# Kernel tuning notes

Measured on AMD Instinct MI355X. Metric: run time of the kernel, lower is better.

Reference implementation:

```python
import jax, jax.numpy as jnp
import numpy as np

NUM_HEADS = 12
T_TASK = 0  # current task index (training uses prompts[:, t:t+1])


def setup_inputs() -> dict:
    key = jax.random.key(0)
    ks = jax.random.split(key, 6)
    B, N, C = 64, 197, 768
    G = 8            # num_selectors
    P = 8            # num_prompts
    NT = 10          # num_tasks
    hd = C // NUM_HEADS
    return {
        "x": jax.random.normal(ks[0], (B, N, C), dtype=jnp.float32),
        "tokens": jax.random.normal(ks[1], (1, B, 1 + G, C), dtype=jnp.float32),
        "qkv_w": jax.random.normal(ks[2], (3 * C, C), dtype=jnp.float32) * 0.02,
        "proj_w": jax.random.normal(ks[3], (C, C), dtype=jnp.float32) * 0.02,
        "proj_b": jax.random.normal(ks[4], (C,), dtype=jnp.float32) * 0.02,
        "prompts": jax.random.normal(ks[5], (2, NT, P, NUM_HEADS, hd), dtype=jnp.float32),
    }


def _forward(x, tokens, qkv_w, proj_w, proj_b, prompts):
    C = x.shape[-1]
    hd = C // NUM_HEADS
    scale = hd ** -0.5
    token_scale = C ** -0.5

    # ---- selector cross-attention (x detached) ----
    xd = jax.lax.stop_gradient(x)
    task_cls = tokens[:, :, 0:1]        # [T,B,1,C]
    selectors = tokens[:, :, 1:]        # [T,B,G,C]
    g_attn = jnp.einsum('tbsc,bnc->tbsn', selectors, xd) * token_scale
    g_soft = jax.nn.softmax(g_attn, axis=-1)
    task_patches = jnp.einsum('bnc,tbsn->tbsc', xd, g_soft)
    task_x = jnp.concatenate([task_cls, task_patches], axis=2)  # [T,B,H,C]
    T, B, H, _ = task_x.shape

    # ---- prompt-augmented task attention ----
    qkv = (task_x @ qkv_w.T).reshape(T, B, H, 3, NUM_HEADS, hd)
    qkv = qkv.transpose(3, 0, 1, 4, 2, 5)          # [3,T,B,heads,H,hd]
    q, k, v = qkv[0], qkv[1], qkv[2]

    pr = prompts[:, T_TASK:T_TASK + 1]             # [2,1,P,heads,hd] (training slice)
    P = pr.shape[2]
    pr = jnp.broadcast_to(pr[:, :, None], (2, 1, B, P, NUM_HEADS, hd))
    pr = pr.transpose(0, 1, 2, 4, 3, 5)            # [2,1,B,heads,P,hd]
    k = jnp.concatenate([pr[0], k], axis=-2)       # [T,B,heads,P+H,hd]
    v = jnp.concatenate([pr[1], v], axis=-2)

    attn = jax.nn.softmax((q @ jnp.swapaxes(k, -2, -1)) * scale, axis=-1)
    out = jnp.swapaxes(attn @ v, 2, 3).reshape(T, B, H, C)
    task_out = out @ proj_w.T + proj_b

    # disable_dandr == False, tome == 0 -> keep selectors, replace cls
    tokens_out = jnp.concatenate([task_out[:, :, 0:1], selectors], axis=2)

    # ---- frozen standard patch attention (no_grad) ----
    Bn, N, _ = x.shape
    qkv2 = (xd @ qkv_w.T).reshape(Bn, N, 3, NUM_HEADS, hd).transpose(2, 0, 3, 1, 4)
    q2, k2, v2 = qkv2[0], qkv2[1], qkv2[2]
    a2 = jax.nn.softmax((q2 @ jnp.swapaxes(k2, -2, -1)) * scale, axis=-1)
    xo = jnp.swapaxes(a2 @ v2, 1, 2).reshape(Bn, N, C)
    xo = jax.lax.stop_gradient(xo @ proj_w.T + proj_b)
    return xo, tokens_out


def reference(x, tokens, qkv_w, proj_w, proj_b, prompts):
    return _forward(x, tokens, qkv_w, proj_w, proj_b, prompts)
```

## Files before the change

### kernel.cpp

```cpp
#include <hip/hip_runtime.h>
#include <hip/hip_bf16.h>
#include <cstddef>
#include <cstdint>


typedef __attribute__((ext_vector_type(8))) short    bf16x8;
typedef __attribute__((ext_vector_type(8))) unsigned short ushort8;
typedef __attribute__((ext_vector_type(4))) unsigned short ushort4v;
typedef __attribute__((ext_vector_type(4))) float    f32x4;

__device__ __forceinline__ unsigned short f2bf_rne(float f) {
    unsigned int u = __float_as_uint(f);
    u += 0x7fff + ((u >> 16) & 1);
    return (unsigned short)(u >> 16);
}
__device__ __forceinline__ float bf2f(unsigned short h) {
    return __uint_as_float(((unsigned int)h) << 16);
}

__global__ __launch_bounds__(256)
void split_hl_kernel(const float* __restrict__ in, unsigned short* __restrict__ hi,
                     unsigned short* __restrict__ lo, int n4)
{
    int i = blockIdx.x * 256 + threadIdx.x;
    const int stride = gridDim.x * 256;
    for (; i < n4; i += stride) {
        float4 v = ((const float4*)in)[i];
        float f[4] = {v.x, v.y, v.z, v.w};
        ushort4v h4, l4;
#pragma unroll
        for (int j = 0; j < 4; ++j) {
            unsigned short hh = f2bf_rne(f[j]);
            h4[j] = hh;
            l4[j] = f2bf_rne(f[j] - bf2f(hh));
        }
        ((ushort4v*)hi)[i] = h4;
        ((ushort4v*)lo)[i] = l4;
    }
}

__global__ __launch_bounds__(256)
void gemm_hl_kernel(const unsigned short* __restrict__ Ah_g, const unsigned short* __restrict__ Al_g,
                    const unsigned short* __restrict__ Bh_g, const unsigned short* __restrict__ Bl_g,
                    const float* __restrict__ bias, float* __restrict__ C,
                    int M, int N, int K)
{
    __shared__ alignas(16) unsigned short As_h[128][32], As_l[128][32];
    __shared__ alignas(16) unsigned short Bs_h[128][32], Bs_l[128][32];

    const int tid = threadIdx.x;
    const int m0 = blockIdx.y * 128;
    const int n0 = blockIdx.x * 128;
    const int wave = tid >> 6, lane = tid & 63;
    const int wr = wave >> 1, wc = wave & 1;
    const int l15 = lane & 15, kg = lane >> 4;

    f32x4 acc[4][4];
#pragma unroll
    for (int i = 0; i < 4; ++i)
#pragma unroll
        for (int j = 0; j < 4; ++j) acc[i][j] = (f32x4){0.f, 0.f, 0.f, 0.f};

    const unsigned short* srcbase =
        (wave == 0) ? Ah_g : (wave == 1) ? Al_g : (wave == 2) ? Bh_g : Bl_g;
    unsigned short* ldsbase =
        (wave == 0) ? &As_h[0][0] : (wave == 1) ? &As_l[0][0]
                                  : (wave == 2) ? &Bs_h[0][0] : &Bs_l[0][0];
    const bool isA = (wave < 2);
    const int rbase = isA ? m0 : n0;
    const int rmax  = isA ? (M - 1) : (N - 1);

    const unsigned short* sp[8];
#pragma unroll
    for (int c = 0; c < 8; ++c) {
        int r = rbase + c * 16 + (lane >> 2);
        if (r > rmax) r = rmax;
        sp[c] = srcbase + (size_t)r * K + (lane & 3) * 8;
    }
    const int loff = (lane >> 2) * 32 + (lane & 3) * 8;

    for (int k0 = 0; k0 < K; k0 += 32) {
        ushort8 stg[8];
#pragma unroll
        for (int c = 0; c < 8; ++c) {
            stg[c] = *(const ushort8*)sp[c];
            sp[c] += 32;
        }
        __syncthreads();
#pragma unroll
        for (int c = 0; c < 8; ++c)
            *(ushort8*)(ldsbase + c * 512 + loff) = stg[c];
        __syncthreads();

        bf16x8 afh[4], afl[4], bfh[4], bfl[4];
#pragma unroll
        for (int f = 0; f < 4; ++f) {
            const int ar = wr * 64 + f * 16 + l15;
            afh[f] = *(const bf16x8*)&As_h[ar][kg * 8];
            afl[f] = *(const bf16x8*)&As_l[ar][kg * 8];
            const int br = wc * 64 + f * 16 + l15;
            bfh[f] = *(const bf16x8*)&Bs_h[br][kg * 8];
            bfl[f] = *(const bf16x8*)&Bs_l[br][kg * 8];
        }
#pragma unroll
        for (int fm = 0; fm < 4; ++fm)
#pragma unroll
            for (int fn = 0; fn < 4; ++fn) {
                acc[fm][fn] = __builtin_amdgcn_mfma_f32_16x16x32_bf16(
                    afh[fm], bfh[fn], acc[fm][fn], 0, 0, 0);
                acc[fm][fn] = __builtin_amdgcn_mfma_f32_16x16x32_bf16(
                    afh[fm], bfl[fn], acc[fm][fn], 0, 0, 0);
                acc[fm][fn] = __builtin_amdgcn_mfma_f32_16x16x32_bf16(
                    afl[fm], bfh[fn], acc[fm][fn], 0, 0, 0);
            }
    }

#pragma unroll
    for (int fm = 0; fm < 4; ++fm)
#pragma unroll
        for (int fn = 0; fn < 4; ++fn) {
            const int col = n0 + wc * 64 + fn * 16 + l15;
            const float bvv = bias ? bias[col] : 0.f;
#pragma unroll
            for (int j = 0; j < 4; ++j) {
                const int row = m0 + wr * 64 + fm * 16 + kg * 4 + j;
                if (row < M) C[(size_t)row * N + col] = acc[fm][fn][j] + bvv;
            }
        }
}

__global__ __launch_bounds__(256)
void task_gather_kernel(const float* __restrict__ x, const float* __restrict__ tokens,
                        unsigned short* __restrict__ tx_hi, unsigned short* __restrict__ tx_lo,
                        float* __restrict__ out_tok)
{
    const int b = blockIdx.x;
    const int tid = threadIdx.x;
    __shared__ float sel[8][772];
    __shared__ float g[8][200];

    for (int l = tid; l < 8 * 192; l += 256) {
        int s = l / 192, c4 = l % 192;
        float4 v = *(const float4*)&tokens[((size_t)b * 9 + 1 + s) * 768 + c4 * 4];
        sel[s][c4 * 4 + 0] = v.x; sel[s][c4 * 4 + 1] = v.y;
        sel[s][c4 * 4 + 2] = v.z; sel[s][c4 * 4 + 3] = v.w;
        *(float4*)&out_tok[((size_t)b * 9 + 1 + s) * 768 + c4 * 4] = v;
    }
    __syncthreads();

    const float token_scale = 0.03608439182435161f;
    for (int idx = tid; idx < 197 * 8; idx += 256) {
        int n = idx >> 3, s = idx & 7;
        const float* xr = &x[((size_t)b * 197 + n) * 768];
        float acc = 0.f;
        for (int c4 = 0; c4 < 192; ++c4) {
            float4 xv = *(const float4*)&xr[c4 * 4];
            acc = fmaf(xv.x, sel[s][c4 * 4 + 0], acc);
            acc = fmaf(xv.y, sel[s][c4 * 4 + 1], acc);
            acc = fmaf(xv.z, sel[s][c4 * 4 + 2], acc);
            acc = fmaf(xv.w, sel[s][c4 * 4 + 3], acc);
        }
        g[s][n] = acc * token_scale;
    }
    __syncthreads();

    const int w = tid >> 6, lane = tid & 63;
    for (int s = w; s < 8; s += 4) {
        float vals[4];
        float m = -1e30f;
#pragma unroll
        for (int t = 0; t < 4; ++t) {
            int n = lane + 64 * t;
            vals[t] = (n < 197) ? g[s][n] : -1e30f;
            m = fmaxf(m, vals[t]);
        }
#pragma unroll
        for (int off = 32; off >= 1; off >>= 1) m = fmaxf(m, __shfl_xor(m, off, 64));
        float sum = 0.f;
#pragma unroll
        for (int t = 0; t < 4; ++t) {
            int n = lane + 64 * t;
            if (n < 197) { vals[t] = __expf(vals[t] - m); sum += vals[t]; }
        }
#pragma unroll
        for (int off = 32; off >= 1; off >>= 1) sum += __shfl_xor(sum, off, 64);
        float inv = 1.f / sum;
#pragma unroll
        for (int t = 0; t < 4; ++t) {
            int n = lane + 64 * t;
            if (n < 197) g[s][n] = vals[t] * inv;
        }
    }
    __syncthreads();

    if (tid < 192) {
        float4 acc8[8];
#pragma unroll
        for (int s = 0; s < 8; ++s) acc8[s] = make_float4(0.f, 0.f, 0.f, 0.f);
        for (int n = 0; n < 197; ++n) {
            float4 xv = *(const float4*)&x[((size_t)b * 197 + n) * 768 + tid * 4];
#pragma unroll
            for (int s = 0; s < 8; ++s) {
                float gw = g[s][n];
                acc8[s].x = fmaf(gw, xv.x, acc8[s].x);
                acc8[s].y = fmaf(gw, xv.y, acc8[s].y);
                acc8[s].z = fmaf(gw, xv.z, acc8[s].z);
                acc8[s].w = fmaf(gw, xv.w, acc8[s].w);
            }
        }
#pragma unroll
        for (int s = 0; s < 8; ++s) {
            float f[4] = {acc8[s].x, acc8[s].y, acc8[s].z, acc8[s].w};
            ushort4v h4, l4;
#pragma unroll
            for (int j = 0; j < 4; ++j) {
                unsigned short hh = f2bf_rne(f[j]);
                h4[j] = hh;
                l4[j] = f2bf_rne(f[j] - bf2f(hh));
            }
            *(ushort4v*)&tx_hi[((size_t)b * 9 + 1 + s) * 768 + tid * 4] = h4;
            *(ushort4v*)&tx_lo[((size_t)b * 9 + 1 + s) * 768 + tid * 4] = l4;
        }
        float4 cls = *(const float4*)&tokens[((size_t)b * 9) * 768 + tid * 4];
        float cf[4] = {cls.x, cls.y, cls.z, cls.w};
        ushort4v h4, l4;
#pragma unroll
        for (int j = 0; j < 4; ++j) {
            unsigned short hh = f2bf_rne(cf[j]);
            h4[j] = hh;
            l4[j] = f2bf_rne(cf[j] - bf2f(hh));
        }
        *(ushort4v*)&tx_hi[((size_t)b * 9) * 768 + tid * 4] = h4;
        *(ushort4v*)&tx_lo[((size_t)b * 9) * 768 + tid * 4] = l4;
    }
}

__global__ __launch_bounds__(256)
void attn_mfma_kernel(const float* __restrict__ qkv2,
                      unsigned short* __restrict__ ao_hi, unsigned short* __restrict__ ao_lo)
{
    __shared__ alignas(16) unsigned short Khi[198][64], Klo[198][64];
    __shared__ alignas(16) unsigned short Vthi[64][232], Vtlo[64][232];
    __shared__ alignas(16) unsigned short Phi[4][16][208], Plo[4][16][208];

    const int h = blockIdx.x, b = blockIdx.y;
    const int tid = threadIdx.x;
    const int wave = tid >> 6, lane = tid & 63;
    const int l15 = lane & 15, kg = lane >> 4;

    const size_t base = (size_t)b * 197 * 2304 + (size_t)h * 64;

    for (int l = tid; l < 197 * 16; l += 256) {
        int n = l >> 4, d4 = l & 15;
        const float* p = &qkv2[base + (size_t)n * 2304 + d4 * 4];
        float4 k4 = *(const float4*)(p + 768);
        float4 v4 = *(const float4*)(p + 1536);
        float kf[4] = {k4.x, k4.y, k4.z, k4.w};
        float vf[4] = {v4.x, v4.y, v4.z, v4.w};
        const int off = (((d4 >> 1) ^ (n & 7)) << 3) + ((d4 & 1) << 2);
        ushort4v kh, kl;
#pragma unroll
        for (int i = 0; i < 4; ++i) {
            unsigned short hh = f2bf_rne(kf[i]);
            kh[i] = hh;
            kl[i] = f2bf_rne(kf[i] - bf2f(hh));
        }
        *(ushort4v*)&Khi[n][off] = kh;
        *(ushort4v*)&Klo[n][off] = kl;
#pragma unroll
        for (int i = 0; i < 4; ++i) {
            unsigned short hh = f2bf_rne(vf[i]);
            Vthi[d4 * 4 + i][n] = hh;
            Vtlo[d4 * 4 + i][n] = f2bf_rne(vf[i] - bf2f(hh));
        }
    }
    for (int l = tid; l < 64 * 11; l += 256) {
        int d = l / 11, c = 197 + l % 11;
        Vthi[d][c] = 0;
        Vtlo[d][c] = 0;
    }
    __syncthreads();

    for (int qt = wave; qt < 13; qt += 4) {
        const int n0 = qt * 16;
        const int qrow = (n0 + l15 < 197) ? (n0 + l15) : 196;

        bf16x8 qh[2], ql[2];
#pragma unroll
        for (int s = 0; s < 2; ++s) {
            const float* qp = &qkv2[base + (size_t)qrow * 2304 + kg * 8 + 32 * s];
            float4 qa = *(const float4*)qp;
            float4 qb = *(const float4*)(qp + 4);
            float qf[8] = {qa.x, qa.y, qa.z, qa.w, qb.x, qb.y, qb.z, qb.w};
#pragma unroll
            for (int i = 0; i < 8; ++i) {
                float v = qf[i] * 0.125f;
                unsigned short hh = f2bf_rne(v);
                qh[s][i] = (short)hh;
                ql[s][i] = (short)f2bf_rne(v - bf2f(hh));
            }
        }

        f32x4 st[13];
#pragma unroll
        for (int t = 0; t < 13; ++t) st[t] = (f32x4){0.f, 0.f, 0.f, 0.f};
#pragma unroll
        for (int t = 0; t < 13; ++t) {
            const int r = 16 * t + l15;
            const bool ok = (t < 12) || (l15 < 5);
#pragma unroll
            for (int s = 0; s < 2; ++s) {
                bf16x8 kh = {0, 0, 0, 0, 0, 0, 0, 0};
                bf16x8 kl = {0, 0, 0, 0, 0, 0, 0, 0};
                if (ok) {
                    const int off = (((kg + 4 * s) ^ (l15 & 7)) << 3);
                    kh = *(const bf16x8*)&Khi[r][off];
                    kl = *(const bf16x8*)&Klo[r][off];
                }
                st[t] = __builtin_amdgcn_mfma_f32_16x16x32_bf16(kh, qh[s], st[t], 0, 0, 0);
                st[t] = __builtin_amdgcn_mfma_f32_16x16x32_bf16(kh, ql[s], st[t], 0, 0, 0);
                st[t] = __builtin_amdgcn_mfma_f32_16x16x32_bf16(kl, qh[s], st[t], 0, 0, 0);
            }
        }

        float m = -1e30f;
#pragma unroll
        for (int t = 0; t < 13; ++t)
#pragma unroll
            for (int j = 0; j < 4; ++j) {
                const int key = 16 * t + kg * 4 + j;
                float v = (key < 197) ? st[t][j] : -1e30f;
                st[t][j] = v;
                m = fmaxf(m, v);
            }
        m = fmaxf(m, __shfl_xor(m, 16, 64));
        m = fmaxf(m, __shfl_xor(m, 32, 64));
        float sum = 0.f;
#pragma unroll
        for (int t = 0; t < 13; ++t)
#pragma unroll
            for (int j = 0; j < 4; ++j) {
                float e = __expf(st[t][j] - m);
                st[t][j] = e;
                sum += e;
            }
        sum += __shfl_xor(sum, 16, 64);
        sum += __shfl_xor(sum, 32, 64);
        const float inv = 1.f / sum;

#pragma unroll
        for (int t = 0; t < 13; ++t) {
            ushort4v ph, pl;
#pragma unroll
            for (int j = 0; j < 4; ++j) {
                unsigned short hh = f2bf_rne(st[t][j]);
                ph[j] = hh;
                pl[j] = f2bf_rne(st[t][j] - bf2f(hh));
            }
            *(ushort4v*)&Phi[wave][l15][16 * t + kg * 4] = ph;
            *(ushort4v*)&Plo[wave][l15][16 * t + kg * 4] = pl;
        }

        f32x4 ao[4];
#pragma unroll
        for (int fd = 0; fd < 4; ++fd) ao[fd] = (f32x4){0.f, 0.f, 0.f, 0.f};
#pragma unroll
        for (int s = 0; s < 7; ++s) {
            const bool act = (s < 6) || (kg < 2);
            bf16x8 ph = {0, 0, 0, 0, 0, 0, 0, 0};
            bf16x8 pl = {0, 0, 0, 0, 0, 0, 0, 0};
            if (act) {
                ph = *(const bf16x8*)&Phi[wave][l15][kg * 8 + 32 * s];
                pl = *(const bf16x8*)&Plo[wave][l15][kg * 8 + 32 * s];
            }
#pragma unroll
            for (int fd = 0; fd < 4; ++fd) {
                bf16x8 vh = {0, 0, 0, 0, 0, 0, 0, 0};
                bf16x8 vl = {0, 0, 0, 0, 0, 0, 0, 0};
                if (act) {
                    vh = *(const bf16x8*)&Vthi[fd * 16 + l15][kg * 8 + 32 * s];
                    vl = *(const bf16x8*)&Vtlo[fd * 16 + l15][kg * 8 + 32 * s];
                }
                ao[fd] = __builtin_amdgcn_mfma_f32_16x16x32_bf16(vh, ph, ao[fd], 0, 0, 0);
                ao[fd] = __builtin_amdgcn_mfma_f32_16x16x32_bf16(vh, pl, ao[fd], 0, 0, 0);
                ao[fd] = __builtin_amdgcn_mfma_f32_16x16x32_bf16(vl, ph, ao[fd], 0, 0, 0);
            }
        }

        if (n0 + l15 < 197) {
            const size_t ob = ((size_t)(b * 197 + n0 + l15)) * 768 + h * 64;
#pragma unroll
            for (int fd = 0; fd < 4; ++fd) {
                ushort4v h4, l4;
#pragma unroll
                for (int j = 0; j < 4; ++j) {
                    float v = ao[fd][j] * inv;
                    unsigned short hh = f2bf_rne(v);
                    h4[j] = hh;
                    l4[j] = f2bf_rne(v - bf2f(hh));
                }
                *(ushort4v*)&ao_hi[ob + fd * 16 + kg * 4] = h4;
                *(ushort4v*)&ao_lo[ob + fd * 16 + kg * 4] = l4;
            }
        }
    }
}

__global__ __launch_bounds__(64)
void task_attn2_kernel(const float* __restrict__ task_qkv, const float* __restrict__ prompts,
                       float* __restrict__ out0)
{
    const int h = blockIdx.x, b = blockIdx.y;
    const int d = threadIdx.x;

    const float q0 = task_qkv[((size_t)b * 9) * 2304 + h * 64 + d] * 0.125f;

    float s[17];
#pragma unroll
    for (int j = 0; j < 17; ++j) {
        float kv = (j < 8)
            ? prompts[(size_t)(j * 12 + h) * 64 + d]
            : task_qkv[((size_t)b * 9 + (j - 8)) * 2304 + 768 + h * 64 + d];
        float prod = q0 * kv;
#pragma unroll
        for (int off = 32; off >= 1; off >>= 1) prod += __shfl_xor(prod, off, 64);
        s[j] = prod;
    }
    float m = s[0];
#pragma unroll
    for (int j = 1; j < 17; ++j) m = fmaxf(m, s[j]);
    float sum = 0.f;
#pragma unroll
    for (int j = 0; j < 17; ++j) { s[j] = __expf(s[j] - m); sum += s[j]; }
    float acc = 0.f;
#pragma unroll
    for (int j = 0; j < 17; ++j) {
        float vv = (j < 8)
            ? prompts[(size_t)61440 + (size_t)(j * 12 + h) * 64 + d]
            : task_qkv[((size_t)b * 9 + (j - 8)) * 2304 + 1536 + h * 64 + d];
        acc = fmaf(s[j], vv, acc);
    }
    out0[((size_t)b * 12 + h) * 64 + d] = acc / sum;
}

__global__ __launch_bounds__(256)
void task_proj_kernel(const float* __restrict__ out0, const float* __restrict__ proj_w,
                      const float* __restrict__ proj_b, float* __restrict__ out_tok)
{
    const int b = blockIdx.x;
    const int col = blockIdx.y * 256 + threadIdx.x;
    __shared__ float xr[768];
    for (int l = threadIdx.x; l < 768; l += 256) xr[l] = out0[(size_t)b * 768 + l];
    __syncthreads();
    const float* wp = &proj_w[(size_t)col * 768];
    float acc = proj_b[col];
    for (int c4 = 0; c4 < 192; ++c4) {
        float4 wv = *(const float4*)&wp[c4 * 4];
        acc = fmaf(wv.x, xr[c4 * 4 + 0], acc);
        acc = fmaf(wv.y, xr[c4 * 4 + 1], acc);
        acc = fmaf(wv.z, xr[c4 * 4 + 2], acc);
        acc = fmaf(wv.w, xr[c4 * 4 + 3], acc);
    }
    out_tok[((size_t)b * 9) * 768 + col] = acc;
}

extern "C" void kernel_launch(void* const* d_in, const int* in_sizes, int n_in,
                              void* d_out, int out_size, void* d_ws, size_t ws_size,
                              hipStream_t stream)
{
    const float* x       = (const float*)d_in[0];
    const float* tokens  = (const float*)d_in[1];
    const float* qkv_w   = (const float*)d_in[2];
    const float* proj_w  = (const float*)d_in[3];
    const float* proj_b  = (const float*)d_in[4];
    const float* prompts = (const float*)d_in[5];

    float* xo      = (float*)d_out;
    float* out_tok = xo + (size_t)12608 * 768;

    float*          qkv2  = (float*)d_ws;
    unsigned short* x_hi  = (unsigned short*)(qkv2 + (size_t)29048832);
    unsigned short* x_lo  = x_hi + (size_t)9682944;
    unsigned short* ao_hi = x_hi;
    unsigned short* ao_lo = x_lo;
    unsigned short* w_hi  = x_lo + (size_t)9682944;
    unsigned short* w_lo  = w_hi + (size_t)1769472;
    unsigned short* pw_hi = w_lo + (size_t)1769472;
    unsigned short* pw_lo = pw_hi + (size_t)589824;
    unsigned short* tx_hi = pw_lo + (size_t)589824;
    unsigned short* tx_lo = tx_hi + (size_t)442368;
    float* task_qkv = (float*)(tx_lo + (size_t)442368);
    float* out0     = task_qkv + (size_t)1327104;

    split_hl_kernel<<<2048, 256, 0, stream>>>(x, x_hi, x_lo, 12608 * 768 / 4);
    split_hl_kernel<<<1728, 256, 0, stream>>>(qkv_w, w_hi, w_lo, 2304 * 768 / 4);
    split_hl_kernel<<<576, 256, 0, stream>>>(proj_w, pw_hi, pw_lo, 768 * 768 / 4);

    task_gather_kernel<<<dim3(64), 256, 0, stream>>>(x, tokens, tx_hi, tx_lo, out_tok);

    gemm_hl_kernel<<<dim3(2304 / 128, (12608 + 127) / 128), 256, 0, stream>>>(
        x_hi, x_lo, w_hi, w_lo, nullptr, qkv2, 12608, 2304, 768);

    attn_mfma_kernel<<<dim3(12, 64), 256, 0, stream>>>(qkv2, ao_hi, ao_lo);

    gemm_hl_kernel<<<dim3(768 / 128, (12608 + 127) / 128), 256, 0, stream>>>(
        ao_hi, ao_lo, pw_hi, pw_lo, proj_b, xo, 12608, 768, 768);

    gemm_hl_kernel<<<dim3(2304 / 128, (576 + 127) / 128), 256, 0, stream>>>(
        tx_hi, tx_lo, w_hi, w_lo, nullptr, task_qkv, 576, 2304, 768);

    task_attn2_kernel<<<dim3(12, 64), 64, 0, stream>>>(task_qkv, prompts, out0);

    task_proj_kernel<<<dim3(64, 3), 256, 0, stream>>>(out0, proj_w, proj_b, out_tok);
}
```

Before: 623.7 us.

## Remap GEMM workgroups per XCD and swizzle LDS tiles to avoid bank conflicts

```diff
diff --git a/kernel.cpp b/kernel.cpp
--- a/kernel.cpp
+++ b/kernel.cpp
@@ -49,8 +49,16 @@
     __shared__ alignas(16) unsigned short Bs_h[128][32], Bs_l[128][32];
 
     const int tid = threadIdx.x;
-    const int m0 = blockIdx.y * 128;
-    const int n0 = blockIdx.x * 128;
+
+    const int nwg  = gridDim.x;
+    const int orig = blockIdx.x;
+    const int q = nwg >> 3, r = nwg & 7;
+    const int xcd = orig & 7, idx = orig >> 3;
+    const int wg = (xcd < r ? xcd * (q + 1) : r * (q + 1) + (xcd - r) * q) + idx;
+    const int NX = N >> 7;
+    const int m0 = (wg / NX) * 128;
+    const int n0 = (wg % NX) * 128;
+
     const int wave = tid >> 6, lane = tid & 63;
     const int wr = wave >> 1, wc = wave & 1;
     const int l15 = lane & 15, kg = lane >> 4;
@@ -73,11 +81,11 @@
     const unsigned short* sp[8];
 #pragma unroll
     for (int c = 0; c < 8; ++c) {
-        int r = rbase + c * 16 + (lane >> 2);
-        if (r > rmax) r = rmax;
-        sp[c] = srcbase + (size_t)r * K + (lane & 3) * 8;
-    }
-    const int loff = (lane >> 2) * 32 + (lane & 3) * 8;
+        int rr = rbase + c * 16 + (lane >> 2);
+        if (rr > rmax) rr = rmax;
+        sp[c] = srcbase + (size_t)rr * K + (lane & 3) * 8;
+    }
+    const int loff = (lane >> 2) * 32 + (((lane & 3) ^ ((lane >> 3) & 3)) * 8);
 
     for (int k0 = 0; k0 < K; k0 += 32) {
         ushort8 stg[8];
@@ -92,15 +100,16 @@
             *(ushort8*)(ldsbase + c * 512 + loff) = stg[c];
         __syncthreads();
 
+        const int rslot = (kg ^ ((l15 >> 1) & 3)) * 8;
         bf16x8 afh[4], afl[4], bfh[4], bfl[4];
 #pragma unroll
         for (int f = 0; f < 4; ++f) {
             const int ar = wr * 64 + f * 16 + l15;
-            afh[f] = *(const bf16x8*)&As_h[ar][kg * 8];
-            afl[f] = *(const bf16x8*)&As_l[ar][kg * 8];
+            afh[f] = *(const bf16x8*)&As_h[ar][rslot];
+            afl[f] = *(const bf16x8*)&As_l[ar][rslot];
             const int br = wc * 64 + f * 16 + l15;
-            bfh[f] = *(const bf16x8*)&Bs_h[br][kg * 8];
-            bfl[f] = *(const bf16x8*)&Bs_l[br][kg * 8];
+            bfh[f] = *(const bf16x8*)&Bs_h[br][rslot];
+            bfl[f] = *(const bf16x8*)&Bs_l[br][rslot];
         }
 #pragma unroll
         for (int fm = 0; fm < 4; ++fm)
@@ -498,15 +507,15 @@
 
     task_gather_kernel<<<dim3(64), 256, 0, stream>>>(x, tokens, tx_hi, tx_lo, out_tok);
 
-    gemm_hl_kernel<<<dim3(2304 / 128, (12608 + 127) / 128), 256, 0, stream>>>(
+    gemm_hl_kernel<<<dim3((2304 / 128) * ((12608 + 127) / 128)), 256, 0, stream>>>(
         x_hi, x_lo, w_hi, w_lo, nullptr, qkv2, 12608, 2304, 768);
 
     attn_mfma_kernel<<<dim3(12, 64), 256, 0, stream>>>(qkv2, ao_hi, ao_lo);
 
-    gemm_hl_kernel<<<dim3(768 / 128, (12608 + 127) / 128), 256, 0, stream>>>(
+    gemm_hl_kernel<<<dim3((768 / 128) * ((12608 + 127) / 128)), 256, 0, stream>>>(
         ao_hi, ao_lo, pw_hi, pw_lo, proj_b, xo, 12608, 768, 768);
 
-    gemm_hl_kernel<<<dim3(2304 / 128, (576 + 127) / 128), 256, 0, stream>>>(
+    gemm_hl_kernel<<<dim3((2304 / 128) * ((576 + 127) / 128)), 256, 0, stream>>>(
         tx_hi, tx_lo, w_hi, w_lo, nullptr, task_qkv, 576, 2304, 768);
 
     task_attn2_kernel<<<dim3(12, 64), 64, 0, stream>>>(task_qkv, prompts, out0);
```

Result: no change. 627.7 us (+0.6%).
